# Kernel optimization log

Hardware: AMD Instinct MI355X
Metric: run time of the kernel (lower is better)

## Reference

```python
import jax, jax.numpy as jnp
import numpy as np

B, T, D, H, O = 1024, 16, 1024, 2048, 1024
BETA, TAU, THR, EPS = 0.9, 2.0, 1.0, 1e-5


def setup_inputs() -> dict:
    key = jax.random.key(0)
    ks = jax.random.split(key, 12)
    def lin(kw, kb, fan_in, fan_out):
        bound = 1.0 / np.sqrt(fan_in)
        W = jax.random.uniform(kw, (fan_in, fan_out), minval=-bound, maxval=bound, dtype=jnp.float32)
        b = jax.random.uniform(kb, (fan_out,), minval=-bound, maxval=bound, dtype=jnp.float32)
        return W, b
    x = jax.random.uniform(ks[0], (B, T, D), dtype=jnp.float32)  # spike-rate-like input, skips encoder
    Wp, bp = lin(ks[1], ks[2], D, H)        # input_proj
    Wfc, bfc = lin(ks[3], ks[4], H, H)      # recursive_layer.fc
    gamma = jnp.ones((H,), jnp.float32)     # recursive_layer.norm
    beta_ln = jnp.zeros((H,), jnp.float32)
    Wg, bg = lin(ks[5], ks[6], H, H)        # controller.gate
    Wenc, benc = lin(ks[7], ks[8], H, H)    # LSA.encoding_weights
    Wrec, brec = lin(ks[9], ks[10], H, H)   # LSA.recurrent_weights
    Wro, bro = lin(ks[11], jax.random.fold_in(key, 99), H, O)  # readout
    return dict(x=x, Wp=Wp, bp=bp, Wfc=Wfc, bfc=bfc, gamma=gamma, beta_ln=beta_ln,
                Wg=Wg, bg=bg, Wenc=Wenc, benc=benc, Wrec=Wrec, brec=brec, Wro=Wro, bro=bro)


def reference(x, Wp, bp, Wfc, bfc, gamma, beta_ln, Wg, bg, Wenc, benc, Wrec, brec, Wro, bro):
    dt = x.dtype
    b = x.shape[0]
    h = Wp.shape[1]

    def ln(v):
        m = v.mean(-1, keepdims=True)
        var = v.var(-1, keepdims=True)  # biased, matches torch LayerNorm
        return (v - m) / jnp.sqrt(var + EPS) * gamma + beta_ln

    # hoist the input projection out of the recurrence: [B,T,D]@[D,H] -> [T,B,H]
    inp_all = jnp.swapaxes(jnp.einsum('btd,dh->bth', x, Wp) + bp, 0, 1)

    def step(carry, inp):
        rec, attr = carry
        # RecursiveMeaningLayer
        update = jnp.tanh(inp @ Wfc + bfc)
        new_rec = BETA * rec + (1.0 - BETA) * update
        ctx = ln(new_rec)
        # RecursionController
        g = jax.nn.sigmoid((ctx + new_rec) @ Wg + bg)
        gated = g * ctx + (1.0 - g) * new_rec
        # LegendreSpikeAttractor
        current = gated @ Wenc + benc + attr @ Wrec + brec
        new_v = attr + (current - attr) / TAU
        spikes = (new_v > THR).astype(dt)
        new_attr = new_v - spikes * THR
        return (new_rec, new_attr), spikes

    init = (jnp.zeros((b, h), dt), jnp.zeros((b, h), dt))
    (rec, attr), spk = jax.lax.scan(step, init, inp_all)  # spk: [T,B,H]
    features = spk.mean(axis=0)
    out = features @ Wro + bro
    return out, rec, attr
```

## Files before the change

kernel.cpp:

```cpp
#include <hip/hip_runtime.h>
#include <math.h>


#define BB 1024
#define TT 16
#define DD 1024
#define HH 2048
#define OO 1024

typedef double d4 __attribute__((ext_vector_type(4)));

struct RdF {
    const float* p; long ld;
    __device__ double operator()(int r, int c) const { return (double)p[(long)r*ld + c]; }
};
struct RdD {
    const double* p; long ld;
    __device__ double operator()(int r, int c) const { return p[(long)r*ld + c]; }
};
struct RdSum {
    const double* a; const double* b; long ld;
    __device__ double operator()(int r, int c) const { long i=(long)r*ld+c; return a[i]+b[i]; }
};
struct RdSpk {
    const float* p; long ld;
    __device__ double operator()(int r, int c) const { return (double)p[(long)r*ld+c] * 0.0625; }
};

#define LDAS 65
#define LDBS 65
#define LDBF 72

template<typename AR>
__device__ __forceinline__ void gemm32(AR A, const float* __restrict__ Bp, long ldb,
                                       int row0, int col0, int kbase, int K,
                                       double* __restrict__ Asd,
                                       float*  __restrict__ Bsf,
                                       d4 acc[2][2])
{
    const int tid  = threadIdx.x;
    const int lane = tid & 63;
    const int wid  = tid >> 6;
    const int wm   = wid >> 1;
    const int wn   = wid & 1;
    const int l15  = lane & 15;
    const int l4   = lane >> 4;
    const int am = tid >> 2, ak = (tid & 3) << 3;
    const int bkb = wid << 3;
    const int brr = lane >> 5;
    const int bc  = (lane & 31) << 1;

    double* A0 = Asd;           double* A1 = Asd + 32*LDAS;
    float*  B0 = Bsf;           float*  B1 = Bsf + 32*LDBF;

    double ar[8]; float2 br[4];
    #pragma unroll
    for (int j = 0; j < 8; ++j) ar[j] = A(row0 + am, kbase + ak + j);
    #pragma unroll
    for (int j = 0; j < 4; ++j) {
        int rw = bkb + 2*j + brr;
        br[j] = *(const float2*)(Bp + (long)(kbase + rw)*ldb + col0 + bc);
    }
    __syncthreads();
    #pragma unroll
    for (int j = 0; j < 8; ++j) A0[(ak + j)*LDAS + am] = ar[j];
    #pragma unroll
    for (int j = 0; j < 4; ++j) {
        int rw = bkb + 2*j + brr;
        *(float2*)(B0 + rw*LDBF + bc) = br[j];
    }
    __syncthreads();

    double *cA = A0, *nA = A1;
    float  *cB = B0, *nB = B1;
    const int nt = K >> 5;
    for (int t = 0; t < nt; ++t) {
        if (t + 1 < nt) {
            #pragma unroll
            for (int j = 0; j < 8; ++j) ar[j] = A(row0 + am, kbase + (t+1)*32 + ak + j);
            #pragma unroll
            for (int j = 0; j < 4; ++j) {
                int rw = bkb + 2*j + brr;
                br[j] = *(const float2*)(Bp + (long)(kbase + (t+1)*32 + rw)*ldb + col0 + bc);
            }
        }
        #pragma unroll
        for (int ks = 0; ks < 8; ++ks) {
            const int kk = ks*4 + l4;
            double a0 = cA[kk*LDAS + wm*32 +      l15];
            double a1 = cA[kk*LDAS + wm*32 + 16 + l15];
            double b0 = (double)cB[kk*LDBF + wn*32 +      l15];
            double b1 = (double)cB[kk*LDBF + wn*32 + 16 + l15];
            acc[0][0] = __builtin_amdgcn_mfma_f64_16x16x4f64(a0, b0, acc[0][0], 0, 0, 0);
            acc[0][1] = __builtin_amdgcn_mfma_f64_16x16x4f64(a0, b1, acc[0][1], 0, 0, 0);
            acc[1][0] = __builtin_amdgcn_mfma_f64_16x16x4f64(a1, b0, acc[1][0], 0, 0, 0);
            acc[1][1] = __builtin_amdgcn_mfma_f64_16x16x4f64(a1, b1, acc[1][1], 0, 0, 0);
        }
        if (t + 1 < nt) {
            #pragma unroll
            for (int j = 0; j < 8; ++j) nA[(ak + j)*LDAS + am] = ar[j];
            #pragma unroll
            for (int j = 0; j < 4; ++j) {
                int rw = bkb + 2*j + brr;
                *(float2*)(nB + rw*LDBF + bc) = br[j];
            }
            __syncthreads();
            double* xd; float* xf;
            xd = cA; cA = nA; nA = xd;
            xf = cB; cB = nB; nB = xf;
        }
    }
}

template<typename AR, typename BR>
__device__ __forceinline__ void gemm64(AR A, BR B, int row0, int col0, int K,
                                       double* __restrict__ Asd,
                                       double* __restrict__ Bsd,
                                       d4 acc[2][2])
{
    const int tid  = threadIdx.x;
    const int lane = tid & 63;
    const int wid  = tid >> 6;
    const int wm   = wid >> 1;
    const int wn   = wid & 1;
    const int l15  = lane & 15;
    const int l4   = lane >> 4;
    const int am = tid >> 2, ak = (tid & 3) << 3;
    const int bk = tid >> 3, bn = (tid & 7) << 3;

    double* A0 = Asd; double* A1 = Asd + 32*LDAS;
    double* B0 = Bsd; double* B1 = Bsd + 32*LDBS;

    double ar[8], br[8];
    #pragma unroll
    for (int j = 0; j < 8; ++j) ar[j] = A(row0 + am, ak + j);
    #pragma unroll
    for (int j = 0; j < 8; ++j) br[j] = B(bk, col0 + bn + j);

    __syncthreads();
    #pragma unroll
    for (int j = 0; j < 8; ++j) A0[(ak + j)*LDAS + am] = ar[j];
    #pragma unroll
    for (int j = 0; j < 8; ++j) B0[bk*LDBS + bn + j] = br[j];
    __syncthreads();

    double *cA = A0, *cB = B0, *nA = A1, *nB = B1;
    const int nt = K >> 5;
    for (int t = 0; t < nt; ++t) {
        if (t + 1 < nt) {
            #pragma unroll
            for (int j = 0; j < 8; ++j) ar[j] = A(row0 + am, (t+1)*32 + ak + j);
            #pragma unroll
            for (int j = 0; j < 8; ++j) br[j] = B((t+1)*32 + bk, col0 + bn + j);
        }
        #pragma unroll
        for (int ks = 0; ks < 8; ++ks) {
            const int kk = ks*4 + l4;
            double a0 = cA[kk*LDAS + wm*32 +      l15];
            double a1 = cA[kk*LDAS + wm*32 + 16 + l15];
            double b0 = cB[kk*LDBS + wn*32 +      l15];
            double b1 = cB[kk*LDBS + wn*32 + 16 + l15];
            acc[0][0] = __builtin_amdgcn_mfma_f64_16x16x4f64(a0, b0, acc[0][0], 0, 0, 0);
            acc[0][1] = __builtin_amdgcn_mfma_f64_16x16x4f64(a0, b1, acc[0][1], 0, 0, 0);
            acc[1][0] = __builtin_amdgcn_mfma_f64_16x16x4f64(a1, b0, acc[1][0], 0, 0, 0);
            acc[1][1] = __builtin_amdgcn_mfma_f64_16x16x4f64(a1, b1, acc[1][1], 0, 0, 0);
        }
        if (t + 1 < nt) {
            #pragma unroll
            for (int j = 0; j < 8; ++j) nA[(ak + j)*LDAS + am] = ar[j];
            #pragma unroll
            for (int j = 0; j < 8; ++j) nB[bk*LDBS + bn + j] = br[j];
            __syncthreads();
            double* x;
            x = cA; cA = nA; nA = x;
            x = cB; cB = nB; nB = x;
        }
    }
}

#define GEMM_EPILOG_VARS                                   \
    const int lane = threadIdx.x & 63;                     \
    const int wid  = threadIdx.x >> 6;                     \
    const int wm   = wid >> 1, wn = wid & 1;               \
    const int l15  = lane & 15, l4 = lane >> 4;

__device__ __forceinline__ void swz3216(int& bx, int& by) {
    int id = bx + (by << 5);
    int k = id & 7, t = id >> 3;
    bx = ((k & 3) << 3) + (t & 7);
    by = ((k >> 2) << 3) + (t >> 3);
}

__global__ __launch_bounds__(256, 3) void k_wpf(const float* __restrict__ Wp,
                                                const float* __restrict__ Wfc,
                                                double* __restrict__ Wpf)
{
    __shared__ double Asd[2*32*LDAS];
    __shared__ float  Bsf[2*32*LDBF];
    d4 acc[2][2] = {};
    int bx = blockIdx.x, by = blockIdx.y;
    swz3216(bx, by);
    int row0 = by*64, col0 = bx*64;
    gemm32(RdF{Wp, HH}, Wfc, HH, row0, col0, 0, HH, Asd, Bsf, acc);
    GEMM_EPILOG_VARS
    #pragma unroll
    for (int i=0;i<2;i++)
      #pragma unroll
      for (int j=0;j<2;j++)
        #pragma unroll
        for (int r=0;r<4;r++) {
            int d = row0 + wm*32 + i*16 + l4 + 4*r;
            int h = col0 + wn*32 + j*16 + l15;
            Wpf[(long)d*HH + h] = acc[i][j][r];
        }
}

__global__ __launch_bounds__(256) void k_bpf(const float* __restrict__ bp,
                                             const float* __restrict__ Wfc,
                                             const float* __restrict__ bfc,
                                             double* __restrict__ bpf)
{
    int h = blockIdx.x*256 + threadIdx.x;
    double acc = 0.0;
    for (int k = 0; k < HH; ++k)
        acc = fma((double)bp[k], (double)Wfc[(long)k*HH + h], acc);
    bpf[h] = acc + (double)bfc[h];
}

__global__ __launch_bounds__(256) void k_update(const float* __restrict__ x, int t,
                                                const double* __restrict__ Wpf,
                                                const double* __restrict__ bpf,
                                                double* __restrict__ rec)
{
    __shared__ double Asd[2*32*LDAS];
    __shared__ double Bsd[2*32*LDBS];
    d4 acc[2][2] = {};
    int bx = blockIdx.x, by = blockIdx.y;
    swz3216(bx, by);
    int row0 = by*64, col0 = bx*64;
    const float* x_t = x + (long)t*DD;
    gemm64(RdF{x_t, (long)TT*DD}, RdD{Wpf, HH}, row0, col0, DD, Asd, Bsd, acc);
    GEMM_EPILOG_VARS
    const double BETA = 0.9;
    const double OMB  = 1.0 - BETA;
    #pragma unroll
    for (int i=0;i<2;i++)
      #pragma unroll
      for (int j=0;j<2;j++)
        #pragma unroll
        for (int r=0;r<4;r++) {
            int b = row0 + wm*32 + i*16 + l4 + 4*r;
            int h = col0 + wn*32 + j*16 + l15;
            double u = tanh(acc[i][j][r] + bpf[h]);
            long idx = (long)b*HH + h;
            rec[idx] = BETA*rec[idx] + OMB*u;
        }
}

__global__ __launch_bounds__(256) void k_ln(const double* __restrict__ rec,
                                            const float* __restrict__ gamma,
                                            const float* __restrict__ beta,
                                            double* __restrict__ ctx)
{
    __shared__ double red[256];
    int b = blockIdx.x, tid = threadIdx.x;
    const double* r = rec + (long)b*HH;
    double s = 0.0;
    for (int h = tid; h < HH; h += 256) s += r[h];
    red[tid] = s; __syncthreads();
    for (int off = 128; off > 0; off >>= 1) {
        if (tid < off) red[tid] += red[tid+off];
        __syncthreads();
    }
    double mean = red[0] / HH;
    __syncthreads();
    double v = 0.0;
    for (int h = tid; h < HH; h += 256) { double d = r[h]-mean; v += d*d; }
    red[tid] = v; __syncthreads();
    for (int off = 128; off > 0; off >>= 1) {
        if (tid < off) red[tid] += red[tid+off];
        __syncthreads();
    }
    double sd = sqrt(red[0] / HH + 1e-5);
    for (int h = tid; h < HH; h += 256) {
        long idx = (long)b*HH + h;
        ctx[idx] = (r[h]-mean)/sd * (double)gamma[h] + (double)beta[h];
    }
}

__global__ __launch_bounds__(256, 3) void k_gate_part(const double* __restrict__ ctx,
                                                      const double* __restrict__ rec,
                                                      const float* __restrict__ Wg,
                                                      double* __restrict__ p0,
                                                      double* __restrict__ p1)
{
    __shared__ double Asd[2*32*LDAS];
    __shared__ float  Bsf[2*32*LDBF];
    d4 acc[2][2] = {};
    int bx = blockIdx.x, by = blockIdx.y, z = blockIdx.z;
    swz3216(bx, by);
    int row0 = by*64, col0 = bx*64;
    gemm32(RdSum{ctx, rec, HH}, Wg, HH, row0, col0, z*1024, 1024, Asd, Bsf, acc);
    double* P = z ? p1 : p0;
    GEMM_EPILOG_VARS
    #pragma unroll
    for (int i=0;i<2;i++)
      #pragma unroll
      for (int j=0;j<2;j++)
        #pragma unroll
        for (int r=0;r<4;r++) {
            int b = row0 + wm*32 + i*16 + l4 + 4*r;
            int h = col0 + wn*32 + j*16 + l15;
            P[(long)b*HH + h] = acc[i][j][r];
        }
}

__global__ __launch_bounds__(256) void k_gatefin(const double* __restrict__ p0,
                                                 const double* __restrict__ ctx,
                                                 const double* __restrict__ rec,
                                                 const float* __restrict__ bg,
                                                 double* __restrict__ gated)
{
    long i = (long)blockIdx.x*256 + threadIdx.x;
    int h = (int)(i & (HH-1));
    double s = p0[i] + gated[i] + (double)bg[h];
    double g = 1.0/(1.0 + exp(-s));
    gated[i] = g*ctx[i] + (1.0-g)*rec[i];
}

__global__ __launch_bounds__(256, 3) void k_current_part(const double* __restrict__ gated,
                                                         const float* __restrict__ Wenc,
                                                         const double* __restrict__ attr_in,
                                                         const float* __restrict__ Wrec,
                                                         double* __restrict__ p0,
                                                         double* __restrict__ p1)
{
    __shared__ double Asd[2*32*LDAS];
    __shared__ float  Bsf[2*32*LDBF];
    d4 acc[2][2] = {};
    int bx = blockIdx.x, by = blockIdx.y, z = blockIdx.z;
    swz3216(bx, by);
    int row0 = by*64, col0 = bx*64;
    const double* Ap = z ? attr_in : gated;
    const float*  Bp = z ? Wrec    : Wenc;
    double*       Cp = z ? p1      : p0;
    gemm32(RdD{Ap, HH}, Bp, HH, row0, col0, 0, HH, Asd, Bsf, acc);
    GEMM_EPILOG_VARS
    #pragma unroll
    for (int i=0;i<2;i++)
      #pragma unroll
      for (int j=0;j<2;j++)
        #pragma unroll
        for (int r=0;r<4;r++) {
            int b = row0 + wm*32 + i*16 + l4 + 4*r;
            int h = col0 + wn*32 + j*16 + l15;
            Cp[(long)b*HH + h] = acc[i][j][r];
        }
}

__global__ __launch_bounds__(256) void k_lif(const double* __restrict__ p0,
                                             const double* __restrict__ attr_in,
                                             const float* __restrict__ benc,
                                             const float* __restrict__ brec,
                                             double* __restrict__ attr_out,
                                             float* __restrict__ spkcnt)
{
    long i = (long)blockIdx.x*256 + threadIdx.x;
    int h = (int)(i & (HH-1));
    const double TAU = 2.0, THR = 1.0;
    double cur = p0[i] + attr_out[i] + (double)benc[h] + (double)brec[h];
    double a   = attr_in[i];
    double nv  = a + (cur - a)/TAU;
    double sp  = (nv > THR) ? 1.0 : 0.0;
    attr_out[i] = nv - sp*THR;
    spkcnt[i] += (float)sp;
}

__global__ __launch_bounds__(256, 3) void k_readout(const float* __restrict__ spkcnt,
                                                    const float* __restrict__ Wro,
                                                    const float* __restrict__ bro,
                                                    float* __restrict__ out)
{
    __shared__ double Asd[2*32*LDAS];
    __shared__ float  Bsf[2*32*LDBF];
    d4 acc[2][2] = {};
    int row0 = blockIdx.y*64, col0 = blockIdx.x*64;
    gemm32(RdSpk{spkcnt, HH}, Wro, OO, row0, col0, 0, HH, Asd, Bsf, acc);
    GEMM_EPILOG_VARS
    #pragma unroll
    for (int i=0;i<2;i++)
      #pragma unroll
      for (int j=0;j<2;j++)
        #pragma unroll
        for (int r=0;r<4;r++) {
            int b = row0 + wm*32 + i*16 + l4 + 4*r;
            int o = col0 + wn*32 + j*16 + l15;
            out[(long)b*OO + o] = (float)(acc[i][j][r] + (double)bro[o]);
        }
}

__global__ __launch_bounds__(256) void k_d2f(const double* __restrict__ src,
                                             float* __restrict__ dst)
{
    long i = (long)blockIdx.x*256 + threadIdx.x;
    dst[i] = (float)src[i];
}

extern "C" void kernel_launch(void* const* d_in, const int* in_sizes, int n_in,
                              void* d_out, int out_size, void* d_ws, size_t ws_size,
                              hipStream_t stream) {
    const float* x    = (const float*)d_in[0];
    const float* Wp   = (const float*)d_in[1];
    const float* bp   = (const float*)d_in[2];
    const float* Wfc  = (const float*)d_in[3];
    const float* bfc  = (const float*)d_in[4];
    const float* gamma= (const float*)d_in[5];
    const float* beta = (const float*)d_in[6];
    const float* Wg   = (const float*)d_in[7];
    const float* bg   = (const float*)d_in[8];
    const float* Wenc = (const float*)d_in[9];
    const float* benc = (const float*)d_in[10];
    const float* Wrec = (const float*)d_in[11];
    const float* brec = (const float*)d_in[12];
    const float* Wro  = (const float*)d_in[13];
    const float* bro  = (const float*)d_in[14];
    float* out = (float*)d_out;

    const long NBH = (long)BB*HH;
    char* p = (char*)d_ws;
    double* Wpf   = (double*)p; p += (long)DD*HH*sizeof(double);
    double* bpf   = (double*)p; p += HH*sizeof(double);
    double* rec   = (double*)p; p += NBH*sizeof(double);
    double* attrA = (double*)p; p += NBH*sizeof(double);
    double* attrB = (double*)p; p += NBH*sizeof(double);
    double* ctx   = (double*)p; p += NBH*sizeof(double);
    double* gated = (double*)p; p += NBH*sizeof(double);
    float*  spkcnt= (float*)p;  p += NBH*sizeof(float);

    hipMemsetAsync(rec,    0, NBH*sizeof(double), stream);
    hipMemsetAsync(attrA,  0, NBH*sizeof(double), stream);
    hipMemsetAsync(spkcnt, 0, NBH*sizeof(float),  stream);

    dim3 blk(256);
    dim3 g_wpf(HH/64, DD/64);
    k_wpf<<<g_wpf, blk, 0, stream>>>(Wp, Wfc, Wpf);
    k_bpf<<<HH/256, blk, 0, stream>>>(bp, Wfc, bfc, bpf);

    dim3 g_step (HH/64, BB/64);
    dim3 g_split(HH/64, BB/64, 2);
    const int NEW = (int)(NBH/256);
    double* ain  = attrA;
    double* aout = attrB;
    for (int t = 0; t < TT; ++t) {
        k_update <<<g_step, blk, 0, stream>>>(x, t, Wpf, bpf, rec);
        k_ln     <<<BB,     blk, 0, stream>>>(rec, gamma, beta, ctx);
        k_gate_part<<<g_split, blk, 0, stream>>>(ctx, rec, Wg, aout, gated);
        k_gatefin  <<<NEW,     blk, 0, stream>>>(aout, ctx, rec, bg, gated);
        k_current_part<<<g_split, blk, 0, stream>>>(gated, Wenc, ain, Wrec, ctx, aout);
        k_lif         <<<NEW,     blk, 0, stream>>>(ctx, ain, benc, brec, aout, spkcnt);
        double* tmp = ain; ain = aout; aout = tmp;
    }

    dim3 g_ro(OO/64, BB/64);
    k_readout<<<g_ro, blk, 0, stream>>>(spkcnt, Wro, bro, out);
    k_d2f<<<NBH/256, blk, 0, stream>>>(rec, out + (long)BB*OO);
    k_d2f<<<NBH/256, blk, 0, stream>>>(ain, out + (long)BB*OO + NBH);
}
```

Measured before the change: 10.02 ms.

## Load GEMM B operand directly to registers and fuse LayerNorm apply into gate GEMM

Replaces the two GEMM helpers with one templated routine that skips shared memory for the B operand. Each lane loads its MFMA B fragments straight from global memory into registers, with prefetch for the next K tile. Shared memory is still used for A. LayerNorm now only writes per-row mean and std, and the normalisation is recomputed inside the gate GEMM's A loader and in the gate finalise kernel, which removes the ctx write and read. Occupancy hints are raised. The risks are uncoalesced, strided global loads for B, B data no longer shared across warps through LDS, and extra divides when the normalisation is recomputed in the A loader.

```diff
diff --git a/kernel.cpp b/kernel.cpp
--- a/kernel.cpp
+++ b/kernel.cpp
@@ -18,9 +18,15 @@
     const double* p; long ld;
     __device__ double operator()(int r, int c) const { return p[(long)r*ld + c]; }
 };
-struct RdSum {
-    const double* a; const double* b; long ld;
-    __device__ double operator()(int r, int c) const { long i=(long)r*ld+c; return a[i]+b[i]; }
+struct RdCR {
+    const double* rec; const double* lnm; const double* lnsd;
+    const float* gamma; const float* beta; long ld;
+    __device__ double operator()(int r, int c) const {
+        long i = (long)r*ld + c;
+        double rv = rec[i];
+        double cv = (rv - lnm[r]) / lnsd[r] * (double)gamma[c] + (double)beta[c];
+        return cv + rv;
+    }
 };
 struct RdSpk {
     const float* p; long ld;
@@ -28,14 +34,11 @@
 };
 
 #define LDAS 65
-#define LDBS 65
-#define LDBF 72
-
-template<typename AR>
-__device__ __forceinline__ void gemm32(AR A, const float* __restrict__ Bp, long ldb,
+
+template<typename AR, typename TB>
+__device__ __forceinline__ void gemmBD(AR A, const TB* __restrict__ Bp, long ldb,
                                        int row0, int col0, int kbase, int K,
                                        double* __restrict__ Asd,
-                                       float*  __restrict__ Bsf,
                                        d4 acc[2][2])
 {
     const int tid  = threadIdx.x;
@@ -46,42 +49,37 @@
     const int l15  = lane & 15;
     const int l4   = lane >> 4;
     const int am = tid >> 2, ak = (tid & 3) << 3;
-    const int bkb = wid << 3;
-    const int brr = lane >> 5;
-    const int bc  = (lane & 31) << 1;
-
-    double* A0 = Asd;           double* A1 = Asd + 32*LDAS;
-    float*  B0 = Bsf;           float*  B1 = Bsf + 32*LDBF;
-
-    double ar[8]; float2 br[4];
+
+    double* A0 = Asd;
+    double* A1 = Asd + 32*LDAS;
+
+    const TB* bB = Bp + (long)(kbase + l4)*ldb + col0 + wn*32 + l15;
+
+    double ar[8];
+    TB bf[16];
     #pragma unroll
     for (int j = 0; j < 8; ++j) ar[j] = A(row0 + am, kbase + ak + j);
     #pragma unroll
-    for (int j = 0; j < 4; ++j) {
-        int rw = bkb + 2*j + brr;
-        br[j] = *(const float2*)(Bp + (long)(kbase + rw)*ldb + col0 + bc);
+    for (int ks = 0; ks < 8; ++ks) {
+        bf[2*ks+0] = bB[(long)(4*ks)*ldb +  0];
+        bf[2*ks+1] = bB[(long)(4*ks)*ldb + 16];
     }
     __syncthreads();
     #pragma unroll
     for (int j = 0; j < 8; ++j) A0[(ak + j)*LDAS + am] = ar[j];
-    #pragma unroll
-    for (int j = 0; j < 4; ++j) {
-        int rw = bkb + 2*j + brr;
-        *(float2*)(B0 + rw*LDBF + bc) = br[j];
-    }
     __syncthreads();
 
     double *cA = A0, *nA = A1;
-    float  *cB = B0, *nB = B1;
     const int nt = K >> 5;
     for (int t = 0; t < nt; ++t) {
+        TB bn_[16];
         if (t + 1 < nt) {
             #pragma unroll
             for (int j = 0; j < 8; ++j) ar[j] = A(row0 + am, kbase + (t+1)*32 + ak + j);
             #pragma unroll
-            for (int j = 0; j < 4; ++j) {
-                int rw = bkb + 2*j + brr;
-                br[j] = *(const float2*)(Bp + (long)(kbase + (t+1)*32 + rw)*ldb + col0 + bc);
+            for (int ks = 0; ks < 8; ++ks) {
+                bn_[2*ks+0] = bB[(long)((t+1)*32 + 4*ks)*ldb +  0];
+                bn_[2*ks+1] = bB[(long)((t+1)*32 + 4*ks)*ldb + 16];
             }
         }
         #pragma unroll
@@ -89,8 +87,8 @@
             const int kk = ks*4 + l4;
             double a0 = cA[kk*LDAS + wm*32 +      l15];
             double a1 = cA[kk*LDAS + wm*32 + 16 + l15];
-            double b0 = (double)cB[kk*LDBF + wn*32 +      l15];
-            double b1 = (double)cB[kk*LDBF + wn*32 + 16 + l15];
+            double b0 = (double)bf[2*ks+0];
+            double b1 = (double)bf[2*ks+1];
             acc[0][0] = __builtin_amdgcn_mfma_f64_16x16x4f64(a0, b0, acc[0][0], 0, 0, 0);
             acc[0][1] = __builtin_amdgcn_mfma_f64_16x16x4f64(a0, b1, acc[0][1], 0, 0, 0);
             acc[1][0] = __builtin_amdgcn_mfma_f64_16x16x4f64(a1, b0, acc[1][0], 0, 0, 0);
@@ -99,81 +97,10 @@
         if (t + 1 < nt) {
             #pragma unroll
             for (int j = 0; j < 8; ++j) nA[(ak + j)*LDAS + am] = ar[j];
+            __syncthreads();
+            double* x = cA; cA = nA; nA = x;
             #pragma unroll
-            for (int j = 0; j < 4; ++j) {
-                int rw = bkb + 2*j + brr;
-                *(float2*)(nB + rw*LDBF + bc) = br[j];
-            }
-            __syncthreads();
-            double* xd; float* xf;
-            xd = cA; cA = nA; nA = xd;
-            xf = cB; cB = nB; nB = xf;
-        }
-    }
-}
-
-template<typename AR, typename BR>
-__device__ __forceinline__ void gemm64(AR A, BR B, int row0, int col0, int K,
-                                       double* __restrict__ Asd,
-                                       double* __restrict__ Bsd,
-                                       d4 acc[2][2])
-{
-    const int tid  = threadIdx.x;
-    const int lane = tid & 63;
-    const int wid  = tid >> 6;
-    const int wm   = wid >> 1;
-    const int wn   = wid & 1;
-    const int l15  = lane & 15;
-    const int l4   = lane >> 4;
-    const int am = tid >> 2, ak = (tid & 3) << 3;
-    const int bk = tid >> 3, bn = (tid & 7) << 3;
-
-    double* A0 = Asd; double* A1 = Asd + 32*LDAS;
-    double* B0 = Bsd; double* B1 = Bsd + 32*LDBS;
-
-    double ar[8], br[8];
-    #pragma unroll
-    for (int j = 0; j < 8; ++j) ar[j] = A(row0 + am, ak + j);
-    #pragma unroll
-    for (int j = 0; j < 8; ++j) br[j] = B(bk, col0 + bn + j);
-
-    __syncthreads();
-    #pragma unroll
-    for (int j = 0; j < 8; ++j) A0[(ak + j)*LDAS + am] = ar[j];
-    #pragma unroll
-    for (int j = 0; j < 8; ++j) B0[bk*LDBS + bn + j] = br[j];
-    __syncthreads();
-
-    double *cA = A0, *cB = B0, *nA = A1, *nB = B1;
-    const int nt = K >> 5;
-    for (int t = 0; t < nt; ++t) {
-        if (t + 1 < nt) {
-            #pragma unroll
-            for (int j = 0; j < 8; ++j) ar[j] = A(row0 + am, (t+1)*32 + ak + j);
-            #pragma unroll
-            for (int j = 0; j < 8; ++j) br[j] = B((t+1)*32 + bk, col0 + bn + j);
-        }
-        #pragma unroll
-        for (int ks = 0; ks < 8; ++ks) {
-            const int kk = ks*4 + l4;
-            double a0 = cA[kk*LDAS + wm*32 +      l15];
-            double a1 = cA[kk*LDAS + wm*32 + 16 + l15];
-            double b0 = cB[kk*LDBS + wn*32 +      l15];
-            double b1 = cB[kk*LDBS + wn*32 + 16 + l15];
-            acc[0][0] = __builtin_amdgcn_mfma_f64_16x16x4f64(a0, b0, acc[0][0], 0, 0, 0);
-            acc[0][1] = __builtin_amdgcn_mfma_f64_16x16x4f64(a0, b1, acc[0][1], 0, 0, 0);
-            acc[1][0] = __builtin_amdgcn_mfma_f64_16x16x4f64(a1, b0, acc[1][0], 0, 0, 0);
-            acc[1][1] = __builtin_amdgcn_mfma_f64_16x16x4f64(a1, b1, acc[1][1], 0, 0, 0);
-        }
-        if (t + 1 < nt) {
-            #pragma unroll
-            for (int j = 0; j < 8; ++j) nA[(ak + j)*LDAS + am] = ar[j];
-            #pragma unroll
-            for (int j = 0; j < 8; ++j) nB[bk*LDBS + bn + j] = br[j];
-            __syncthreads();
-            double* x;
-            x = cA; cA = nA; nA = x;
-            x = cB; cB = nB; nB = x;
+            for (int q = 0; q < 16; ++q) bf[q] = bn_[q];
         }
     }
 }
@@ -191,17 +118,16 @@
     by = ((k >> 2) << 3) + (t >> 3);
 }
 
-__global__ __launch_bounds__(256, 3) void k_wpf(const float* __restrict__ Wp,
+__global__ __launch_bounds__(256, 4) void k_wpf(const float* __restrict__ Wp,
                                                 const float* __restrict__ Wfc,
                                                 double* __restrict__ Wpf)
 {
     __shared__ double Asd[2*32*LDAS];
-    __shared__ float  Bsf[2*32*LDBF];
     d4 acc[2][2] = {};
     int bx = blockIdx.x, by = blockIdx.y;
     swz3216(bx, by);
     int row0 = by*64, col0 = bx*64;
-    gemm32(RdF{Wp, HH}, Wfc, HH, row0, col0, 0, HH, Asd, Bsf, acc);
+    gemmBD(RdF{Wp, HH}, Wfc, HH, row0, col0, 0, HH, Asd, acc);
     GEMM_EPILOG_VARS
     #pragma unroll
     for (int i=0;i<2;i++)
@@ -227,19 +153,18 @@
     bpf[h] = acc + (double)bfc[h];
 }
 
-__global__ __launch_bounds__(256) void k_update(const float* __restrict__ x, int t,
-                                                const double* __restrict__ Wpf,
-                                                const double* __restrict__ bpf,
-                                                double* __restrict__ rec)
+__global__ __launch_bounds__(256, 2) void k_update(const float* __restrict__ x, int t,
+                                                   const double* __restrict__ Wpf,
+                                                   const double* __restrict__ bpf,
+                                                   double* __restrict__ rec)
 {
     __shared__ double Asd[2*32*LDAS];
-    __shared__ double Bsd[2*32*LDBS];
     d4 acc[2][2] = {};
     int bx = blockIdx.x, by = blockIdx.y;
     swz3216(bx, by);
     int row0 = by*64, col0 = bx*64;
     const float* x_t = x + (long)t*DD;
-    gemm64(RdF{x_t, (long)TT*DD}, RdD{Wpf, HH}, row0, col0, DD, Asd, Bsd, acc);
+    gemmBD(RdF{x_t, (long)TT*DD}, Wpf, (long)HH, row0, col0, 0, DD, Asd, acc);
     GEMM_EPILOG_VARS
     const double BETA = 0.9;
     const double OMB  = 1.0 - BETA;
@@ -257,10 +182,9 @@
         }
 }
 
-__global__ __launch_bounds__(256) void k_ln(const double* __restrict__ rec,
-                                            const float* __restrict__ gamma,
-                                            const float* __restrict__ beta,
-                                            double* __restrict__ ctx)
+__global__ __launch_bounds__(256) void k_lnstat(const double* __restrict__ rec,
+                                                double* __restrict__ lnm,
+                                                double* __restrict__ lnsd)
 {
     __shared__ double red[256];
     int b = blockIdx.x, tid = threadIdx.x;
@@ -281,26 +205,28 @@
         if (tid < off) red[tid] += red[tid+off];
         __syncthreads();
     }
-    double sd = sqrt(red[0] / HH + 1e-5);
-    for (int h = tid; h < HH; h += 256) {
-        long idx = (long)b*HH + h;
-        ctx[idx] = (r[h]-mean)/sd * (double)gamma[h] + (double)beta[h];
-    }
-}
-
-__global__ __launch_bounds__(256, 3) void k_gate_part(const double* __restrict__ ctx,
-                                                      const double* __restrict__ rec,
+    if (tid == 0) {
+        lnm[b]  = mean;
+        lnsd[b] = sqrt(red[0] / HH + 1e-5);
+    }
+}
+
+__global__ __launch_bounds__(256, 4) void k_gate_part(const double* __restrict__ rec,
+                                                      const double* __restrict__ lnm,
+                                                      const double* __restrict__ lnsd,
+                                                      const float* __restrict__ gamma,
+                                                      const float* __restrict__ beta,
                                                       const float* __restrict__ Wg,
                                                       double* __restrict__ p0,
                                                       double* __restrict__ p1)
 {
     __shared__ double Asd[2*32*LDAS];
-    __shared__ float  Bsf[2*32*LDBF];
     d4 acc[2][2] = {};
     int bx = blockIdx.x, by = blockIdx.y, z = blockIdx.z;
     swz3216(bx, by);
     int row0 = by*64, col0 = bx*64;
-    gemm32(RdSum{ctx, rec, HH}, Wg, HH, row0, col0, z*1024, 1024, Asd, Bsf, acc);
+    gemmBD(RdCR{rec, lnm, lnsd, gamma, beta, HH}, Wg, (long)HH,
+           row0, col0, z*1024, 1024, Asd, acc);
     double* P = z ? p1 : p0;
     GEMM_EPILOG_VARS
     #pragma unroll
@@ -316,19 +242,25 @@
 }
 
 __global__ __launch_bounds__(256) void k_gatefin(const double* __restrict__ p0,
-                                                 const double* __restrict__ ctx,
                                                  const double* __restrict__ rec,
+                                                 const double* __restrict__ lnm,
+                                                 const double* __restrict__ lnsd,
+                                                 const float* __restrict__ gamma,
+                                                 const float* __restrict__ beta,
                                                  const float* __restrict__ bg,
                                                  double* __restrict__ gated)
 {
     long i = (long)blockIdx.x*256 + threadIdx.x;
-    int h = (int)(i & (HH-1));
+    int h   = (int)(i & (HH-1));
+    int row = (int)(i >> 11);
+    double rv = rec[i];
+    double cv = (rv - lnm[row]) / lnsd[row] * (double)gamma[h] + (double)beta[h];
     double s = p0[i] + gated[i] + (double)bg[h];
     double g = 1.0/(1.0 + exp(-s));
-    gated[i] = g*ctx[i] + (1.0-g)*rec[i];
-}
-
-__global__ __launch_bounds__(256, 3) void k_current_part(const double* __restrict__ gated,
+    gated[i] = g*cv + (1.0-g)*rv;
+}
+
+__global__ __launch_bounds__(256, 4) void k_current_part(const double* __restrict__ gated,
                                                          const float* __restrict__ Wenc,
                                                          const double* __restrict__ attr_in,
                                                          const float* __restrict__ Wrec,
@@ -336,7 +268,6 @@
                                                          double* __restrict__ p1)
 {
     __shared__ double Asd[2*32*LDAS];
-    __shared__ float  Bsf[2*32*LDBF];
     d4 acc[2][2] = {};
     int bx = blockIdx.x, by = blockIdx.y, z = blockIdx.z;
     swz3216(bx, by);
@@ -344,7 +275,7 @@
     const double* Ap = z ? attr_in : gated;
     const float*  Bp = z ? Wrec    : Wenc;
     double*       Cp = z ? p1      : p0;
-    gemm32(RdD{Ap, HH}, Bp, HH, row0, col0, 0, HH, Asd, Bsf, acc);
+    gemmBD(RdD{Ap, HH}, Bp, (long)HH, row0, col0, 0, HH, Asd, acc);
     GEMM_EPILOG_VARS
     #pragma unroll
     for (int i=0;i<2;i++)
@@ -376,16 +307,15 @@
     spkcnt[i] += (float)sp;
 }
 
-__global__ __launch_bounds__(256, 3) void k_readout(const float* __restrict__ spkcnt,
+__global__ __launch_bounds__(256, 4) void k_readout(const float* __restrict__ spkcnt,
                                                     const float* __restrict__ Wro,
                                                     const float* __restrict__ bro,
                                                     float* __restrict__ out)
 {
     __shared__ double Asd[2*32*LDAS];
-    __shared__ float  Bsf[2*32*LDBF];
     d4 acc[2][2] = {};
     int row0 = blockIdx.y*64, col0 = blockIdx.x*64;
-    gemm32(RdSpk{spkcnt, HH}, Wro, OO, row0, col0, 0, HH, Asd, Bsf, acc);
+    gemmBD(RdSpk{spkcnt, HH}, Wro, (long)OO, row0, col0, 0, HH, Asd, acc);
     GEMM_EPILOG_VARS
     #pragma unroll
     for (int i=0;i<2;i++)
@@ -436,6 +366,8 @@
     double* ctx   = (double*)p; p += NBH*sizeof(double);
     double* gated = (double*)p; p += NBH*sizeof(double);
     float*  spkcnt= (float*)p;  p += NBH*sizeof(float);
+    double* lnm   = (double*)p; p += BB*sizeof(double);
+    double* lnsd  = (double*)p; p += BB*sizeof(double);
 
     hipMemsetAsync(rec,    0, NBH*sizeof(double), stream);
     hipMemsetAsync(attrA,  0, NBH*sizeof(double), stream);
@@ -453,9 +385,9 @@
     double* aout = attrB;
     for (int t = 0; t < TT; ++t) {
         k_update <<<g_step, blk, 0, stream>>>(x, t, Wpf, bpf, rec);
-        k_ln     <<<BB,     blk, 0, stream>>>(rec, gamma, beta, ctx);
-        k_gate_part<<<g_split, blk, 0, stream>>>(ctx, rec, Wg, aout, gated);
-        k_gatefin  <<<NEW,     blk, 0, stream>>>(aout, ctx, rec, bg, gated);
+        k_lnstat <<<BB,     blk, 0, stream>>>(rec, lnm, lnsd);
+        k_gate_part<<<g_split, blk, 0, stream>>>(rec, lnm, lnsd, gamma, beta, Wg, aout, gated);
+        k_gatefin  <<<NEW,     blk, 0, stream>>>(aout, rec, lnm, lnsd, gamma, beta, bg, gated);
         k_current_part<<<g_split, blk, 0, stream>>>(gated, Wenc, ain, Wrec, ctx, aout);
         k_lif         <<<NEW,     blk, 0, stream>>>(ctx, ain, benc, brec, aout, spkcnt);
         double* tmp = ain; ain = aout; aout = tmp;
```

After: 9.858 ms. No clear change (-1.6%).
